# Kernel tuning notes

Measured on AMD Instinct MI355X. Metric: run time of the kernel, lower is better.

The kernel has to match this reference:

```python
import jax, jax.numpy as jnp
import numpy as np

N, E = 8192, 65536
IN_C, OUT_C, EF = 64, 16, 8
L1, L2 = 48, 32  # in - floor((in-out)/3), in - floor(2*(in-out)/3)


def setup_inputs() -> dict:
    key = jax.random.key(0)
    ks = jax.random.split(key, 10)
    rn = lambda k, shape, s: jax.random.normal(k, shape, dtype=jnp.float32) * s
    return {
        "x": jax.random.normal(ks[0], (N, IN_C), dtype=jnp.float32),
        "edge_index": jax.random.randint(ks[1], (2, E), 0, N, dtype=jnp.int32),
        "edge_attr": jax.random.normal(ks[2], (E, EF), dtype=jnp.float32),
        "nn1_w": rn(ks[3], (EF, IN_C * L1), 0.05),
        "nn1_b": jnp.zeros((IN_C * L1,), jnp.float32),
        "root1": rn(ks[4], (IN_C, L1), 0.1),
        "bias1": jnp.zeros((L1,), jnp.float32),
        "nn2_w": rn(ks[5], (EF, L1 * L2), 0.05),
        "nn2_b": jnp.zeros((L1 * L2,), jnp.float32),
        "root2": rn(ks[6], (L1, L2), 0.1),
        "bias2": jnp.zeros((L2,), jnp.float32),
        "mu_w": rn(ks[7], (L2, OUT_C), 0.1),
        "mu_b": jnp.zeros((OUT_C,), jnp.float32),
        "ls_w": rn(ks[8], (L2, OUT_C), 0.1),
        "ls_b": jnp.zeros((OUT_C,), jnp.float32),
    }


def _nnconv(x, src, dst, edge_attr, nn_w, nn_b, root, bias, c_in, c_out):
    # edge MLP -> per-edge weight matrices [E, c_in, c_out]
    w = (edge_attr @ nn_w + nn_b).reshape(-1, c_in, c_out)
    msg = jnp.einsum('ei,eio->eo', x[src], w)  # gather + per-edge matvec
    agg = jax.ops.segment_sum(msg, dst, num_segments=x.shape[0])  # sum aggregation
    return agg + x @ root + bias  # root transform + bias


def _gcn(x, src, dst, w, b):
    n = x.shape[0]
    # degree over target nodes, including self-loop (edge_weight = 1)
    deg = jax.ops.segment_sum(jnp.ones_like(src, jnp.float32), dst, num_segments=n) + 1.0
    dinv = jax.lax.rsqrt(deg)
    h = x @ w
    norm = dinv[src] * dinv[dst]  # [E]
    agg = jax.ops.segment_sum(h[src] * norm[:, None], dst, num_segments=n)
    return agg + h * (1.0 / deg)[:, None] + b  # self-loop contribution: deg_i^{-1}


def reference(x, edge_index, edge_attr, nn1_w, nn1_b, root1, bias1,
              nn2_w, nn2_b, root2, bias2, mu_w, mu_b, ls_w, ls_b):
    src, dst = edge_index[0], edge_index[1]
    h = jax.nn.relu(_nnconv(x, src, dst, edge_attr, nn1_w, nn1_b, root1, bias1, IN_C, L1))
    h = jax.nn.relu(_nnconv(h, src, dst, edge_attr, nn2_w, nn2_b, root2, bias2, L1, L2))
    return (_gcn(h, src, dst, mu_w, mu_b), _gcn(h, src, dst, ls_w, ls_b))
```

## Files before the change

kernel.cpp:

```cpp
#include <hip/hip_runtime.h>

#define NN 8192
#define EE 65536
#define IN_C 64
#define L1C 48
#define L2C 32
#define OUT_C 16
#define EF 8

#define T1_COLS 480
#define T2_COLS 320

__global__ __launch_bounds__(256) void k_T1(const float* __restrict__ x,
                                            const float* __restrict__ w,
                                            const float* __restrict__ b,
                                            const float* __restrict__ root,
                                            float* __restrict__ T1) {
    __shared__ float xsT[64 * 16];
    const int n0 = blockIdx.x * 16;
    for (int t = threadIdx.x; t < 16 * 64; t += 256) {
        int n = t >> 6, i = t & 63;
        xsT[i * 16 + n] = x[(n0 + n) * 64 + i];
    }
    __syncthreads();
    for (int c = threadIdx.x; c < T1_COLS; c += 256) {
        int f = c / 48, o = c - f * 48;
        const float* wp;
        if (f < 8)      wp = w + f * 3072 + o;
        else if (f == 8) wp = b + o;
        else             wp = root + o;
        float acc[16];
#pragma unroll
        for (int n = 0; n < 16; n++) acc[n] = 0.f;
#pragma unroll 16
        for (int i = 0; i < 64; i++) {
            float wv = wp[i * 48];
            const float* xr = &xsT[i * 16];
#pragma unroll
            for (int n = 0; n < 16; n++) acc[n] += xr[n] * wv;
        }
#pragma unroll
        for (int n = 0; n < 16; n++) T1[(size_t)(n0 + n) * T1_COLS + c] = acc[n];
    }
}

__global__ __launch_bounds__(256) void k_T2(const float* __restrict__ h1,
                                            const float* __restrict__ w,
                                            const float* __restrict__ b,
                                            const float* __restrict__ root,
                                            float* __restrict__ T2) {
    __shared__ float xsT[48 * 16];
    const int n0 = blockIdx.x * 16;
    for (int t = threadIdx.x; t < 16 * 48; t += 256) {
        int n = t / 48, i = t - n * 48;
        xsT[i * 16 + n] = h1[(n0 + n) * 48 + i];
    }
    __syncthreads();
    for (int c = threadIdx.x; c < T2_COLS; c += 256) {
        int f = c >> 5, o = c & 31;
        const float* wp;
        if (f < 8)      wp = w + f * 1536 + o;
        else if (f == 8) wp = b + o;
        else             wp = root + o;
        float acc[16];
#pragma unroll
        for (int n = 0; n < 16; n++) acc[n] = 0.f;
#pragma unroll 16
        for (int i = 0; i < 48; i++) {
            float wv = wp[i * 32];
            const float* xr = &xsT[i * 16];
#pragma unroll
            for (int n = 0; n < 16; n++) acc[n] += xr[n] * wv;
        }
#pragma unroll
        for (int n = 0; n < 16; n++) T2[(size_t)(n0 + n) * T2_COLS + c] = acc[n];
    }
}

__global__ __launch_bounds__(256) void k_zero(float* __restrict__ p, int n4) {
    int i = blockIdx.x * 256 + threadIdx.x;
    if (i < n4) ((float4*)p)[i] = make_float4(0.f, 0.f, 0.f, 0.f);
}

__global__ __launch_bounds__(256) void k_edge1(const int* __restrict__ ei,
                                               const float* __restrict__ ea,
                                               const float* __restrict__ T1,
                                               float* __restrict__ agg1) {
    int idx = blockIdx.x * 256 + threadIdx.x;
    int e = idx / 48, o = idx - e * 48;
    if (e >= EE) return;
    int s = ei[e], d = ei[EE + e];
    const float* t = T1 + (size_t)s * T1_COLS + o;
    const float4* a4 = (const float4*)(ea + (size_t)e * 8);
    float4 a0 = a4[0], a1 = a4[1];
    float m = t[384];
    m += a0.x * t[0 * 48];
    m += a0.y * t[1 * 48];
    m += a0.z * t[2 * 48];
    m += a0.w * t[3 * 48];
    m += a1.x * t[4 * 48];
    m += a1.y * t[5 * 48];
    m += a1.z * t[6 * 48];
    m += a1.w * t[7 * 48];
    atomicAdd(agg1 + (size_t)d * 48 + o, m);
}

__global__ __launch_bounds__(256) void k_h1(const float* __restrict__ agg1,
                                            const float* __restrict__ T1,
                                            const float* __restrict__ bias1,
                                            float* __restrict__ h1) {
    int idx = blockIdx.x * 256 + threadIdx.x;
    if (idx >= NN * 48) return;
    int n = idx / 48, o = idx - n * 48;
    float v = agg1[idx] + T1[(size_t)n * T1_COLS + 432 + o] + bias1[o];
    h1[idx] = v > 0.f ? v : 0.f;
}

__global__ __launch_bounds__(256) void k_edge2(const int* __restrict__ ei,
                                               const float* __restrict__ ea,
                                               const float* __restrict__ T2,
                                               float* __restrict__ agg2,
                                               float* __restrict__ deg) {
    int idx = blockIdx.x * 256 + threadIdx.x;
    int e = idx >> 5, o = idx & 31;
    if (e >= EE) return;
    int s = ei[e], d = ei[EE + e];
    const float* t = T2 + (size_t)s * T2_COLS + o;
    const float4* a4 = (const float4*)(ea + (size_t)e * 8);
    float4 a0 = a4[0], a1 = a4[1];
    float m = t[256];
    m += a0.x * t[0 * 32];
    m += a0.y * t[1 * 32];
    m += a0.z * t[2 * 32];
    m += a0.w * t[3 * 32];
    m += a1.x * t[4 * 32];
    m += a1.y * t[5 * 32];
    m += a1.z * t[6 * 32];
    m += a1.w * t[7 * 32];
    atomicAdd(agg2 + (size_t)d * 32 + o, m);
    if (o == 0) atomicAdd(deg + d, 1.0f);
}

__global__ __launch_bounds__(256) void k_post(const float* __restrict__ agg2,
                                              const float* __restrict__ T2,
                                              const float* __restrict__ bias2,
                                              const float* __restrict__ mu_w,
                                              const float* __restrict__ mu_b,
                                              const float* __restrict__ ls_w,
                                              const float* __restrict__ ls_b,
                                              const float* __restrict__ deg,
                                              float* __restrict__ hmu,
                                              float* __restrict__ hls,
                                              float* __restrict__ dinv,
                                              float* __restrict__ out) {
    __shared__ float h2s[8][32];
    const int n0 = blockIdx.x * 8;
    const int lid = threadIdx.x >> 5;
    const int o = threadIdx.x & 31;
    const int n = n0 + lid;
    float v = agg2[(size_t)n * 32 + o] + T2[(size_t)n * T2_COLS + 288 + o] + bias2[o];
    v = v > 0.f ? v : 0.f;
    h2s[lid][o] = v;
    __syncthreads();
    const float* wm = (o < 16) ? mu_w : ls_w;
    const float* bb = (o < 16) ? mu_b : ls_b;
    const int oo = o & 15;
    float acc = 0.f;
#pragma unroll
    for (int i = 0; i < 32; i++) acc += h2s[lid][i] * wm[i * 16 + oo];
    float d = deg[n] + 1.0f;
    float di = rsqrtf(d);
    if (o == 0) dinv[n] = di;
    float init = acc / d + bb[oo];
    if (o < 16) {
        hmu[(size_t)n * 16 + oo] = acc;
        out[(size_t)n * 16 + oo] = init;
    } else {
        hls[(size_t)n * 16 + oo] = acc;
        out[(size_t)NN * 16 + (size_t)n * 16 + oo] = init;
    }
}

__global__ __launch_bounds__(256) void k_gcn_edge(const int* __restrict__ ei,
                                                  const float* __restrict__ hmu,
                                                  const float* __restrict__ hls,
                                                  const float* __restrict__ dinv,
                                                  float* __restrict__ out) {
    int idx = blockIdx.x * 256 + threadIdx.x;
    int e = idx >> 4, o = idx & 15;
    if (e >= EE) return;
    int s = ei[e], d = ei[EE + e];
    float norm = dinv[s] * dinv[d];
    atomicAdd(out + (size_t)d * 16 + o, hmu[(size_t)s * 16 + o] * norm);
    atomicAdd(out + (size_t)NN * 16 + (size_t)d * 16 + o, hls[(size_t)s * 16 + o] * norm);
}

extern "C" void kernel_launch(void* const* d_in, const int* in_sizes, int n_in,
                              void* d_out, int out_size, void* d_ws, size_t ws_size,
                              hipStream_t stream) {
    const float* x     = (const float*)d_in[0];
    const int*   ei    = (const int*)d_in[1];
    const float* ea    = (const float*)d_in[2];
    const float* nn1_w = (const float*)d_in[3];
    const float* nn1_b = (const float*)d_in[4];
    const float* root1 = (const float*)d_in[5];
    const float* bias1 = (const float*)d_in[6];
    const float* nn2_w = (const float*)d_in[7];
    const float* nn2_b = (const float*)d_in[8];
    const float* root2 = (const float*)d_in[9];
    const float* bias2 = (const float*)d_in[10];
    const float* mu_w  = (const float*)d_in[11];
    const float* mu_b  = (const float*)d_in[12];
    const float* ls_w  = (const float*)d_in[13];
    const float* ls_b  = (const float*)d_in[14];
    float* out = (float*)d_out;

    float* W    = (float*)d_ws;
    float* T1   = W;
    float* T2   = W;
    float* agg1 = W + 3932160;
    float* agg2 = agg1 + 393216;
    float* deg  = agg2 + 262144;
    float* h1   = deg + 8192;
    float* hmu  = h1 + 393216;
    float* hls  = hmu + 131072;
    float* dinv = hls + 131072;

    k_T1<<<dim3(NN / 16), dim3(256), 0, stream>>>(x, nn1_w, nn1_b, root1, T1);
    k_zero<<<dim3((165888 + 255) / 256), dim3(256), 0, stream>>>(agg1, 165888);
    k_edge1<<<dim3((EE * 48) / 256), dim3(256), 0, stream>>>(ei, ea, T1, agg1);
    k_h1<<<dim3((NN * 48) / 256), dim3(256), 0, stream>>>(agg1, T1, bias1, h1);
    k_T2<<<dim3(NN / 16), dim3(256), 0, stream>>>(h1, nn2_w, nn2_b, root2, T2);
    k_edge2<<<dim3((EE * 32) / 256), dim3(256), 0, stream>>>(ei, ea, T2, agg2, deg);
    k_post<<<dim3(NN / 8), dim3(256), 0, stream>>>(agg2, T2, bias2, mu_w, mu_b,
                                                   ls_w, ls_b, deg, hmu, hls, dinv, out);
    k_gcn_edge<<<dim3((EE * 16) / 256), dim3(256), 0, stream>>>(ei, hmu, hls, dinv, out);
}
```

Before: 157.9 us.

## Prepack weights, fuse zero/ReLU kernels, vectorize edge kernels with float4

Adds a pre-kernel that zeroes the accumulators and repacks the edge-MLP, bias and root weights into contiguous row-major matrices. The node-transform GEMMs are restructured so each thread holds one node's features in registers and computes 32 output columns with uniform weight loads. The h1 ReLU kernel is fused into the T2 GEMM prologue, and T2 gets its own buffer instead of aliasing T1. The edge and GCN scatter kernels now use one thread per four channels with float4 gathers, cutting thread count and index loads, but they still issue scalar atomics and each thread carries more registers.

```diff
diff --git a/kernel.cpp b/kernel.cpp
--- a/kernel.cpp
+++ b/kernel.cpp
@@ -2,84 +2,116 @@
 
 #define NN 8192
 #define EE 65536
-#define IN_C 64
-#define L1C 48
-#define L2C 32
-#define OUT_C 16
-#define EF 8
-
 #define T1_COLS 480
 #define T2_COLS 320
 
+__global__ __launch_bounds__(256) void k_pre(const float* __restrict__ w1,
+                                             const float* __restrict__ b1,
+                                             const float* __restrict__ r1,
+                                             const float* __restrict__ w2,
+                                             const float* __restrict__ b2,
+                                             const float* __restrict__ r2,
+                                             float* __restrict__ Wp1,
+                                             float* __restrict__ Wp2,
+                                             float* __restrict__ zbase) {
+    int t = blockIdx.x * 256 + threadIdx.x;
+    if (t < 165888) {
+        ((float4*)zbase)[t] = make_float4(0.f, 0.f, 0.f, 0.f);
+        return;
+    }
+    int p = t - 165888;
+    if (p < 30720) {
+        int i = p / 480, c = p - i * 480;
+        float v;
+        if (c < 384) { int f = c / 48, o = c - f * 48; v = w1[f * 3072 + i * 48 + o]; }
+        else if (c < 432) v = b1[i * 48 + (c - 384)];
+        else              v = r1[i * 48 + (c - 432)];
+        Wp1[p] = v;
+    } else {
+        p -= 30720;
+        int i = p / 320, c = p - i * 320;
+        float v;
+        if (c < 256) { int f = c >> 5, o = c & 31; v = w2[f * 1536 + i * 32 + o]; }
+        else if (c < 288) v = b2[i * 32 + (c - 256)];
+        else              v = r2[i * 32 + (c - 288)];
+        Wp2[p] = v;
+    }
+}
+
 __global__ __launch_bounds__(256) void k_T1(const float* __restrict__ x,
-                                            const float* __restrict__ w,
-                                            const float* __restrict__ b,
-                                            const float* __restrict__ root,
+                                            const float* __restrict__ Wp,
                                             float* __restrict__ T1) {
-    __shared__ float xsT[64 * 16];
-    const int n0 = blockIdx.x * 16;
-    for (int t = threadIdx.x; t < 16 * 64; t += 256) {
-        int n = t >> 6, i = t & 63;
-        xsT[i * 16 + n] = x[(n0 + n) * 64 + i];
-    }
-    __syncthreads();
-    for (int c = threadIdx.x; c < T1_COLS; c += 256) {
-        int f = c / 48, o = c - f * 48;
-        const float* wp;
-        if (f < 8)      wp = w + f * 3072 + o;
-        else if (f == 8) wp = b + o;
-        else             wp = root + o;
+    const int j = blockIdx.x * 4 + (threadIdx.x >> 6);
+    const int lane = threadIdx.x & 63;
+    const int nt = j / 15, grp = j - nt * 15;
+    const int n = nt * 64 + lane;
+    float xr[64];
+    const float4* xp = (const float4*)(x + (size_t)n * 64);
+#pragma unroll
+    for (int q = 0; q < 16; q++) {
+        float4 v = xp[q];
+        xr[4 * q] = v.x; xr[4 * q + 1] = v.y; xr[4 * q + 2] = v.z; xr[4 * q + 3] = v.w;
+    }
+#pragma unroll
+    for (int ch = 0; ch < 2; ch++) {
+        const int c0 = grp * 32 + ch * 16;
+        const float* wr = Wp + c0;
         float acc[16];
 #pragma unroll
-        for (int n = 0; n < 16; n++) acc[n] = 0.f;
-#pragma unroll 16
+        for (int c = 0; c < 16; c++) acc[c] = 0.f;
+#pragma unroll
         for (int i = 0; i < 64; i++) {
-            float wv = wp[i * 48];
-            const float* xr = &xsT[i * 16];
-#pragma unroll
-            for (int n = 0; n < 16; n++) acc[n] += xr[n] * wv;
+            float xv = xr[i];
+#pragma unroll
+            for (int c = 0; c < 16; c++) acc[c] += xv * wr[i * 480 + c];
         }
-#pragma unroll
-        for (int n = 0; n < 16; n++) T1[(size_t)(n0 + n) * T1_COLS + c] = acc[n];
-    }
-}
-
-__global__ __launch_bounds__(256) void k_T2(const float* __restrict__ h1,
-                                            const float* __restrict__ w,
-                                            const float* __restrict__ b,
-                                            const float* __restrict__ root,
+        float4* o4 = (float4*)(T1 + (size_t)n * 480 + c0);
+#pragma unroll
+        for (int q = 0; q < 4; q++)
+            o4[q] = make_float4(acc[4 * q], acc[4 * q + 1], acc[4 * q + 2], acc[4 * q + 3]);
+    }
+}
+
+__global__ __launch_bounds__(256) void k_T2(const float* __restrict__ agg1,
+                                            const float* __restrict__ T1,
+                                            const float* __restrict__ bias1,
+                                            const float* __restrict__ Wp,
                                             float* __restrict__ T2) {
-    __shared__ float xsT[48 * 16];
-    const int n0 = blockIdx.x * 16;
-    for (int t = threadIdx.x; t < 16 * 48; t += 256) {
-        int n = t / 48, i = t - n * 48;
-        xsT[i * 16 + n] = h1[(n0 + n) * 48 + i];
-    }
-    __syncthreads();
-    for (int c = threadIdx.x; c < T2_COLS; c += 256) {
-        int f = c >> 5, o = c & 31;
-        const float* wp;
-        if (f < 8)      wp = w + f * 1536 + o;
-        else if (f == 8) wp = b + o;
-        else             wp = root + o;
+    const int j = blockIdx.x * 4 + (threadIdx.x >> 6);
+    const int lane = threadIdx.x & 63;
+    const int nt = j / 10, grp = j - nt * 10;
+    const int n = nt * 64 + lane;
+    float xr[48];
+    const float4* ap = (const float4*)(agg1 + (size_t)n * 48);
+    const float4* rp = (const float4*)(T1 + (size_t)n * 480 + 432);
+#pragma unroll
+    for (int q = 0; q < 12; q++) {
+        float4 a = ap[q];
+        float4 r = rp[q];
+        float4 b = *(const float4*)(bias1 + 4 * q);
+        xr[4 * q]     = fmaxf(a.x + r.x + b.x, 0.f);
+        xr[4 * q + 1] = fmaxf(a.y + r.y + b.y, 0.f);
+        xr[4 * q + 2] = fmaxf(a.z + r.z + b.z, 0.f);
+        xr[4 * q + 3] = fmaxf(a.w + r.w + b.w, 0.f);
+    }
+#pragma unroll
+    for (int ch = 0; ch < 2; ch++) {
+        const int c0 = grp * 32 + ch * 16;
+        const float* wr = Wp + c0;
         float acc[16];
 #pragma unroll
-        for (int n = 0; n < 16; n++) acc[n] = 0.f;
-#pragma unroll 16
+        for (int c = 0; c < 16; c++) acc[c] = 0.f;
+#pragma unroll
         for (int i = 0; i < 48; i++) {
-            float wv = wp[i * 32];
-            const float* xr = &xsT[i * 16];
-#pragma unroll
-            for (int n = 0; n < 16; n++) acc[n] += xr[n] * wv;
+            float xv = xr[i];
+#pragma unroll
+            for (int c = 0; c < 16; c++) acc[c] += xv * wr[i * 320 + c];
         }
-#pragma unroll
-        for (int n = 0; n < 16; n++) T2[(size_t)(n0 + n) * T2_COLS + c] = acc[n];
-    }
-}
-
-__global__ __launch_bounds__(256) void k_zero(float* __restrict__ p, int n4) {
-    int i = blockIdx.x * 256 + threadIdx.x;
-    if (i < n4) ((float4*)p)[i] = make_float4(0.f, 0.f, 0.f, 0.f);
+        float4* o4 = (float4*)(T2 + (size_t)n * 320 + c0);
+#pragma unroll
+        for (int q = 0; q < 4; q++)
+            o4[q] = make_float4(acc[4 * q], acc[4 * q + 1], acc[4 * q + 2], acc[4 * q + 3]);
+    }
 }
 
 __global__ __launch_bounds__(256) void k_edge1(const int* __restrict__ ei,
@@ -87,33 +119,27 @@
                                                const float* __restrict__ T1,
                                                float* __restrict__ agg1) {
     int idx = blockIdx.x * 256 + threadIdx.x;
-    int e = idx / 48, o = idx - e * 48;
+    int e = idx / 12, o4 = idx - e * 12;
     if (e >= EE) return;
     int s = ei[e], d = ei[EE + e];
-    const float* t = T1 + (size_t)s * T1_COLS + o;
+    const float* t = T1 + (size_t)s * 480 + o4 * 4;
     const float4* a4 = (const float4*)(ea + (size_t)e * 8);
     float4 a0 = a4[0], a1 = a4[1];
-    float m = t[384];
-    m += a0.x * t[0 * 48];
-    m += a0.y * t[1 * 48];
-    m += a0.z * t[2 * 48];
-    m += a0.w * t[3 * 48];
-    m += a1.x * t[4 * 48];
-    m += a1.y * t[5 * 48];
-    m += a1.z * t[6 * 48];
-    m += a1.w * t[7 * 48];
-    atomicAdd(agg1 + (size_t)d * 48 + o, m);
-}
-
-__global__ __launch_bounds__(256) void k_h1(const float* __restrict__ agg1,
-                                            const float* __restrict__ T1,
-                                            const float* __restrict__ bias1,
-                                            float* __restrict__ h1) {
-    int idx = blockIdx.x * 256 + threadIdx.x;
-    if (idx >= NN * 48) return;
-    int n = idx / 48, o = idx - n * 48;
-    float v = agg1[idx] + T1[(size_t)n * T1_COLS + 432 + o] + bias1[o];
-    h1[idx] = v > 0.f ? v : 0.f;
+    float4 m = *(const float4*)(t + 384);
+    float4 w;
+    w = *(const float4*)(t + 0 * 48); m.x += a0.x * w.x; m.y += a0.x * w.y; m.z += a0.x * w.z; m.w += a0.x * w.w;
+    w = *(const float4*)(t + 1 * 48); m.x += a0.y * w.x; m.y += a0.y * w.y; m.z += a0.y * w.z; m.w += a0.y * w.w;
+    w = *(const float4*)(t + 2 * 48); m.x += a0.z * w.x; m.y += a0.z * w.y; m.z += a0.z * w.z; m.w += a0.z * w.w;
+    w = *(const float4*)(t + 3 * 48); m.x += a0.w * w.x; m.y += a0.w * w.y; m.z += a0.w * w.z; m.w += a0.w * w.w;
+    w = *(const float4*)(t + 4 * 48); m.x += a1.x * w.x; m.y += a1.x * w.y; m.z += a1.x * w.z; m.w += a1.x * w.w;
+    w = *(const float4*)(t + 5 * 48); m.x += a1.y * w.x; m.y += a1.y * w.y; m.z += a1.y * w.z; m.w += a1.y * w.w;
+    w = *(const float4*)(t + 6 * 48); m.x += a1.z * w.x; m.y += a1.z * w.y; m.z += a1.z * w.z; m.w += a1.z * w.w;
+    w = *(const float4*)(t + 7 * 48); m.x += a1.w * w.x; m.y += a1.w * w.y; m.z += a1.w * w.z; m.w += a1.w * w.w;
+    float* ag = agg1 + (size_t)d * 48 + o4 * 4;
+    atomicAdd(ag + 0, m.x);
+    atomicAdd(ag + 1, m.y);
+    atomicAdd(ag + 2, m.z);
+    atomicAdd(ag + 3, m.w);
 }
 
 __global__ __launch_bounds__(256) void k_edge2(const int* __restrict__ ei,
@@ -122,23 +148,28 @@
                                                float* __restrict__ agg2,
                                                float* __restrict__ deg) {
     int idx = blockIdx.x * 256 + threadIdx.x;
-    int e = idx >> 5, o = idx & 31;
+    int e = idx >> 3, o4 = idx & 7;
     if (e >= EE) return;
     int s = ei[e], d = ei[EE + e];
-    const float* t = T2 + (size_t)s * T2_COLS + o;
+    const float* t = T2 + (size_t)s * 320 + o4 * 4;
     const float4* a4 = (const float4*)(ea + (size_t)e * 8);
     float4 a0 = a4[0], a1 = a4[1];
-    float m = t[256];
-    m += a0.x * t[0 * 32];
-    m += a0.y * t[1 * 32];
-    m += a0.z * t[2 * 32];
-    m += a0.w * t[3 * 32];
-    m += a1.x * t[4 * 32];
-    m += a1.y * t[5 * 32];
-    m += a1.z * t[6 * 32];
-    m += a1.w * t[7 * 32];
-    atomicAdd(agg2 + (size_t)d * 32 + o, m);
-    if (o == 0) atomicAdd(deg + d, 1.0f);
+    float4 m = *(const float4*)(t + 256);
+    float4 w;
+    w = *(const float4*)(t + 0 * 32); m.x += a0.x * w.x; m.y += a0.x * w.y; m.z += a0.x * w.z; m.w += a0.x * w.w;
+    w = *(const float4*)(t + 1 * 32); m.x += a0.y * w.x; m.y += a0.y * w.y; m.z += a0.y * w.z; m.w += a0.y * w.w;
+    w = *(const float4*)(t + 2 * 32); m.x += a0.z * w.x; m.y += a0.z * w.y; m.z += a0.z * w.z; m.w += a0.z * w.w;
+    w = *(const float4*)(t + 3 * 32); m.x += a0.w * w.x; m.y += a0.w * w.y; m.z += a0.w * w.z; m.w += a0.w * w.w;
+    w = *(const float4*)(t + 4 * 32); m.x += a1.x * w.x; m.y += a1.x * w.y; m.z += a1.x * w.z; m.w += a1.x * w.w;
+    w = *(const float4*)(t + 5 * 32); m.x += a1.y * w.x; m.y += a1.y * w.y; m.z += a1.y * w.z; m.w += a1.y * w.w;
+    w = *(const float4*)(t + 6 * 32); m.x += a1.z * w.x; m.y += a1.z * w.y; m.z += a1.z * w.z; m.w += a1.z * w.w;
+    w = *(const float4*)(t + 7 * 32); m.x += a1.w * w.x; m.y += a1.w * w.y; m.z += a1.w * w.z; m.w += a1.w * w.w;
+    float* ag = agg2 + (size_t)d * 32 + o4 * 4;
+    atomicAdd(ag + 0, m.x);
+    atomicAdd(ag + 1, m.y);
+    atomicAdd(ag + 2, m.z);
+    atomicAdd(ag + 3, m.w);
+    if (o4 == 0) atomicAdd(deg + d, 1.0f);
 }
 
 __global__ __launch_bounds__(256) void k_post(const float* __restrict__ agg2,
@@ -158,9 +189,8 @@
     const int lid = threadIdx.x >> 5;
     const int o = threadIdx.x & 31;
     const int n = n0 + lid;
-    float v = agg2[(size_t)n * 32 + o] + T2[(size_t)n * T2_COLS + 288 + o] + bias2[o];
-    v = v > 0.f ? v : 0.f;
-    h2s[lid][o] = v;
+    float v = agg2[(size_t)n * 32 + o] + T2[(size_t)n * 320 + 288 + o] + bias2[o];
+    h2s[lid][o] = v > 0.f ? v : 0.f;
     __syncthreads();
     const float* wm = (o < 16) ? mu_w : ls_w;
     const float* bb = (o < 16) ? mu_b : ls_b;
@@ -187,12 +217,22 @@
                                                   const float* __restrict__ dinv,
                                                   float* __restrict__ out) {
     int idx = blockIdx.x * 256 + threadIdx.x;
-    int e = idx >> 4, o = idx & 15;
+    int e = idx >> 2, o4 = idx & 3;
     if (e >= EE) return;
     int s = ei[e], d = ei[EE + e];
     float norm = dinv[s] * dinv[d];
-    atomicAdd(out + (size_t)d * 16 + o, hmu[(size_t)s * 16 + o] * norm);
-    atomicAdd(out + (size_t)NN * 16 + (size_t)d * 16 + o, hls[(size_t)s * 16 + o] * norm);
+    float4 m = *(const float4*)(hmu + (size_t)s * 16 + o4 * 4);
+    float4 l = *(const float4*)(hls + (size_t)s * 16 + o4 * 4);
+    float* om = out + (size_t)d * 16 + o4 * 4;
+    float* ol = out + (size_t)NN * 16 + (size_t)d * 16 + o4 * 4;
+    atomicAdd(om + 0, m.x * norm);
+    atomicAdd(om + 1, m.y * norm);
+    atomicAdd(om + 2, m.z * norm);
+    atomicAdd(om + 3, m.w * norm);
+    atomicAdd(ol + 0, l.x * norm);
+    atomicAdd(ol + 1, l.y * norm);
+    atomicAdd(ol + 2, l.z * norm);
+    atomicAdd(ol + 3, l.w * norm);
 }
 
 extern "C" void kernel_launch(void* const* d_in, const int* in_sizes, int n_in,
@@ -216,23 +256,25 @@
     float* out = (float*)d_out;
 
     float* W    = (float*)d_ws;
-    float* T1   = W;
-    float* T2   = W;
-    float* agg1 = W + 3932160;
+    float* Wp1  = W;
+    float* Wp2  = Wp1 + 30720;
+    float* T1   = Wp2 + 15360;
+    float* T2   = T1 + 3932160;
+    float* agg1 = T2 + 2621440;
     float* agg2 = agg1 + 393216;
     float* deg  = agg2 + 262144;
-    float* h1   = deg + 8192;
-    float* hmu  = h1 + 393216;
+    float* hmu  = deg + 8192;
     float* hls  = hmu + 131072;
     float* dinv = hls + 131072;
 
-    k_T1<<<dim3(NN / 16), dim3(256), 0, stream>>>(x, nn1_w, nn1_b, root1, T1);
-    k_zero<<<dim3((165888 + 255) / 256), dim3(256), 0, stream>>>(agg1, 165888);
-    k_edge1<<<dim3((EE * 48) / 256), dim3(256), 0, stream>>>(ei, ea, T1, agg1);
-    k_h1<<<dim3((NN * 48) / 256), dim3(256), 0, stream>>>(agg1, T1, bias1, h1);
-    k_T2<<<dim3(NN / 16), dim3(256), 0, stream>>>(h1, nn2_w, nn2_b, root2, T2);
-    k_edge2<<<dim3((EE * 32) / 256), dim3(256), 0, stream>>>(ei, ea, T2, agg2, deg);
+    k_pre<<<dim3(828), dim3(256), 0, stream>>>(nn1_w, nn1_b, root1,
+                                               nn2_w, nn2_b, root2,
+                                               Wp1, Wp2, agg1);
+    k_T1<<<dim3(480), dim3(256), 0, stream>>>(x, Wp1, T1);
+    k_edge1<<<dim3((EE * 12) / 256), dim3(256), 0, stream>>>(ei, ea, T1, agg1);
+    k_T2<<<dim3(320), dim3(256), 0, stream>>>(agg1, T1, bias1, Wp2, T2);
+    k_edge2<<<dim3((EE * 8) / 256), dim3(256), 0, stream>>>(ei, ea, T2, agg2, deg);
     k_post<<<dim3(NN / 8), dim3(256), 0, stream>>>(agg2, T2, bias2, mu_w, mu_b,
                                                    ls_w, ls_b, deg, hmu, hls, dinv, out);
-    k_gcn_edge<<<dim3((EE * 16) / 256), dim3(256), 0, stream>>>(ei, hmu, hls, dinv, out);
-}
+    k_gcn_edge<<<dim3((EE * 4) / 256), dim3(256), 0, stream>>>(ei, hmu, hls, dinv, out);
+}
```

Measured after the change: 274.7 us. 74.0% more time.

## Rebuild NNConv as CSR gather of edge-feature outer products then dense GEMM

Applied to the files above, without the earlier changes.

Replaces the atomic scatter pipeline with a CSR built on device (histogram, scan, scatter). Each NNConv first aggregates per-destination sums of edge_attr times source features (plus a plain sum and the self row), then applies one dense GEMM against the stacked weight, bias and root matrix. The GCN is also made atomic-free via CSR gather, and the mu/ls heads are fused with layer 2. This removes float atomics and the large per-source T tables, at the cost of several small extra kernels, including a single-block scan, and a large Z workspace.

```diff
diff --git a/kernel.cpp b/kernel.cpp
--- a/kernel.cpp
+++ b/kernel.cpp
@@ -2,197 +2,278 @@
 
 #define NN 8192
 #define EE 65536
-#define IN_C 64
-#define L1C 48
-#define L2C 32
-#define OUT_C 16
-#define EF 8
-
-#define T1_COLS 480
-#define T2_COLS 320
-
-__global__ __launch_bounds__(256) void k_T1(const float* __restrict__ x,
-                                            const float* __restrict__ w,
-                                            const float* __restrict__ b,
-                                            const float* __restrict__ root,
-                                            float* __restrict__ T1) {
-    __shared__ float xsT[64 * 16];
-    const int n0 = blockIdx.x * 16;
-    for (int t = threadIdx.x; t < 16 * 64; t += 256) {
-        int n = t >> 6, i = t & 63;
-        xsT[i * 16 + n] = x[(n0 + n) * 64 + i];
-    }
+
+__global__ __launch_bounds__(256) void k_pre(const float* __restrict__ w1,
+                                             const float* __restrict__ b1,
+                                             const float* __restrict__ r1,
+                                             const float* __restrict__ w2,
+                                             const float* __restrict__ b2,
+                                             const float* __restrict__ r2,
+                                             float* __restrict__ Wf1,
+                                             float* __restrict__ Wf2,
+                                             int* __restrict__ cnt) {
+    int t = blockIdx.x * 256 + threadIdx.x;
+    if (t < 8192) { cnt[t] = 0; return; }
+    t -= 8192;
+    if (t < 30720) {
+        float v;
+        if (t < 24576)      v = w1[t];
+        else if (t < 27648) v = b1[t - 24576];
+        else                v = r1[t - 27648];
+        Wf1[t] = v;
+        return;
+    }
+    t -= 30720;
+    float v;
+    if (t < 12288)      v = w2[t];
+    else if (t < 13824) v = b2[t - 12288];
+    else                v = r2[t - 13824];
+    Wf2[t] = v;
+}
+
+__global__ __launch_bounds__(256) void k_hist(const int* __restrict__ ei,
+                                              int* __restrict__ cnt) {
+    int e = blockIdx.x * 256 + threadIdx.x;
+    atomicAdd(&cnt[ei[EE + e]], 1);
+}
+
+__global__ __launch_bounds__(1024) void k_scan(const int* __restrict__ cnt,
+                                               int* __restrict__ row_ptr,
+                                               int* __restrict__ cursor) {
+    __shared__ int sd[1024];
+    const int t = threadIdx.x;
+    const int base = t * 8;
+    int v[8];
+    int s = 0;
+#pragma unroll
+    for (int j = 0; j < 8; j++) { v[j] = cnt[base + j]; s += v[j]; }
+    sd[t] = s;
     __syncthreads();
-    for (int c = threadIdx.x; c < T1_COLS; c += 256) {
-        int f = c / 48, o = c - f * 48;
-        const float* wp;
-        if (f < 8)      wp = w + f * 3072 + o;
-        else if (f == 8) wp = b + o;
-        else             wp = root + o;
-        float acc[16];
-#pragma unroll
-        for (int n = 0; n < 16; n++) acc[n] = 0.f;
-#pragma unroll 16
-        for (int i = 0; i < 64; i++) {
-            float wv = wp[i * 48];
-            const float* xr = &xsT[i * 16];
-#pragma unroll
-            for (int n = 0; n < 16; n++) acc[n] += xr[n] * wv;
-        }
-#pragma unroll
-        for (int n = 0; n < 16; n++) T1[(size_t)(n0 + n) * T1_COLS + c] = acc[n];
-    }
-}
-
-__global__ __launch_bounds__(256) void k_T2(const float* __restrict__ h1,
-                                            const float* __restrict__ w,
-                                            const float* __restrict__ b,
-                                            const float* __restrict__ root,
-                                            float* __restrict__ T2) {
-    __shared__ float xsT[48 * 16];
-    const int n0 = blockIdx.x * 16;
-    for (int t = threadIdx.x; t < 16 * 48; t += 256) {
-        int n = t / 48, i = t - n * 48;
-        xsT[i * 16 + n] = h1[(n0 + n) * 48 + i];
-    }
-    __syncthreads();
-    for (int c = threadIdx.x; c < T2_COLS; c += 256) {
-        int f = c >> 5, o = c & 31;
-        const float* wp;
-        if (f < 8)      wp = w + f * 1536 + o;
-        else if (f == 8) wp = b + o;
-        else             wp = root + o;
-        float acc[16];
-#pragma unroll
-        for (int n = 0; n < 16; n++) acc[n] = 0.f;
-#pragma unroll 16
-        for (int i = 0; i < 48; i++) {
-            float wv = wp[i * 32];
-            const float* xr = &xsT[i * 16];
-#pragma unroll
-            for (int n = 0; n < 16; n++) acc[n] += xr[n] * wv;
-        }
-#pragma unroll
-        for (int n = 0; n < 16; n++) T2[(size_t)(n0 + n) * T2_COLS + c] = acc[n];
-    }
-}
-
-__global__ __launch_bounds__(256) void k_zero(float* __restrict__ p, int n4) {
-    int i = blockIdx.x * 256 + threadIdx.x;
-    if (i < n4) ((float4*)p)[i] = make_float4(0.f, 0.f, 0.f, 0.f);
-}
-
-__global__ __launch_bounds__(256) void k_edge1(const int* __restrict__ ei,
-                                               const float* __restrict__ ea,
-                                               const float* __restrict__ T1,
-                                               float* __restrict__ agg1) {
-    int idx = blockIdx.x * 256 + threadIdx.x;
-    int e = idx / 48, o = idx - e * 48;
-    if (e >= EE) return;
-    int s = ei[e], d = ei[EE + e];
-    const float* t = T1 + (size_t)s * T1_COLS + o;
-    const float4* a4 = (const float4*)(ea + (size_t)e * 8);
-    float4 a0 = a4[0], a1 = a4[1];
-    float m = t[384];
-    m += a0.x * t[0 * 48];
-    m += a0.y * t[1 * 48];
-    m += a0.z * t[2 * 48];
-    m += a0.w * t[3 * 48];
-    m += a1.x * t[4 * 48];
-    m += a1.y * t[5 * 48];
-    m += a1.z * t[6 * 48];
-    m += a1.w * t[7 * 48];
-    atomicAdd(agg1 + (size_t)d * 48 + o, m);
-}
-
-__global__ __launch_bounds__(256) void k_h1(const float* __restrict__ agg1,
-                                            const float* __restrict__ T1,
+    for (int off = 1; off < 1024; off <<= 1) {
+        int a = sd[t];
+        int b = (t >= off) ? sd[t - off] : 0;
+        __syncthreads();
+        sd[t] = a + b;
+        __syncthreads();
+    }
+    int run = sd[t] - s;
+#pragma unroll
+    for (int j = 0; j < 8; j++) {
+        row_ptr[base + j] = run;
+        cursor[base + j] = run;
+        run += v[j];
+    }
+    if (t == 1023) row_ptr[8192] = run;
+}
+
+__global__ __launch_bounds__(256) void k_scatter(const int* __restrict__ ei,
+                                                 int* __restrict__ cursor,
+                                                 int* __restrict__ cs_e) {
+    int e = blockIdx.x * 256 + threadIdx.x;
+    int d = ei[EE + e];
+    int slot = atomicAdd(&cursor[d], 1);
+    cs_e[slot] = e;
+}
+
+__global__ __launch_bounds__(256) void k_y1(const int* __restrict__ ei,
+                                            const float* __restrict__ ea,
+                                            const float* __restrict__ x,
+                                            const int* __restrict__ row_ptr,
+                                            const int* __restrict__ cs_e,
+                                            float* __restrict__ Z1) {
+    const int lane = threadIdx.x & 63;
+    const int d = blockIdx.x * 4 + (threadIdx.x >> 6);
+    float y[9];
+#pragma unroll
+    for (int f = 0; f < 9; f++) y[f] = 0.f;
+    const int rp0 = row_ptr[d], rp1 = row_ptr[d + 1];
+    for (int idx = rp0; idx < rp1; idx++) {
+        int e = cs_e[idx];
+        int s = ei[e];
+        float xv = x[(size_t)s * 64 + lane];
+        float4 a0 = *(const float4*)(ea + (size_t)e * 8);
+        float4 a1 = *(const float4*)(ea + (size_t)e * 8 + 4);
+        y[0] += a0.x * xv; y[1] += a0.y * xv; y[2] += a0.z * xv; y[3] += a0.w * xv;
+        y[4] += a1.x * xv; y[5] += a1.y * xv; y[6] += a1.z * xv; y[7] += a1.w * xv;
+        y[8] += xv;
+    }
+    float* zr = Z1 + (size_t)d * 640;
+#pragma unroll
+    for (int f = 0; f < 9; f++) zr[f * 64 + lane] = y[f];
+    zr[576 + lane] = x[(size_t)d * 64 + lane];
+}
+
+__global__ __launch_bounds__(192) void k_g1(const float* __restrict__ Z1,
+                                            const float* __restrict__ Wf1,
                                             const float* __restrict__ bias1,
                                             float* __restrict__ h1) {
-    int idx = blockIdx.x * 256 + threadIdx.x;
-    if (idx >= NN * 48) return;
-    int n = idx / 48, o = idx - n * 48;
-    float v = agg1[idx] + T1[(size_t)n * T1_COLS + 432 + o] + bias1[o];
-    h1[idx] = v > 0.f ? v : 0.f;
-}
-
-__global__ __launch_bounds__(256) void k_edge2(const int* __restrict__ ei,
-                                               const float* __restrict__ ea,
-                                               const float* __restrict__ T2,
-                                               float* __restrict__ agg2,
-                                               float* __restrict__ deg) {
-    int idx = blockIdx.x * 256 + threadIdx.x;
-    int e = idx >> 5, o = idx & 31;
-    if (e >= EE) return;
-    int s = ei[e], d = ei[EE + e];
-    const float* t = T2 + (size_t)s * T2_COLS + o;
-    const float4* a4 = (const float4*)(ea + (size_t)e * 8);
-    float4 a0 = a4[0], a1 = a4[1];
-    float m = t[256];
-    m += a0.x * t[0 * 32];
-    m += a0.y * t[1 * 32];
-    m += a0.z * t[2 * 32];
-    m += a0.w * t[3 * 32];
-    m += a1.x * t[4 * 32];
-    m += a1.y * t[5 * 32];
-    m += a1.z * t[6 * 32];
-    m += a1.w * t[7 * 32];
-    atomicAdd(agg2 + (size_t)d * 32 + o, m);
-    if (o == 0) atomicAdd(deg + d, 1.0f);
-}
-
-__global__ __launch_bounds__(256) void k_post(const float* __restrict__ agg2,
-                                              const float* __restrict__ T2,
-                                              const float* __restrict__ bias2,
-                                              const float* __restrict__ mu_w,
-                                              const float* __restrict__ mu_b,
-                                              const float* __restrict__ ls_w,
-                                              const float* __restrict__ ls_b,
-                                              const float* __restrict__ deg,
-                                              float* __restrict__ hmu,
-                                              float* __restrict__ hls,
-                                              float* __restrict__ dinv,
-                                              float* __restrict__ out) {
-    __shared__ float h2s[8][32];
-    const int n0 = blockIdx.x * 8;
-    const int lid = threadIdx.x >> 5;
-    const int o = threadIdx.x & 31;
-    const int n = n0 + lid;
-    float v = agg2[(size_t)n * 32 + o] + T2[(size_t)n * T2_COLS + 288 + o] + bias2[o];
-    v = v > 0.f ? v : 0.f;
-    h2s[lid][o] = v;
+    __shared__ float Zs[64 * 32];
+    __shared__ float Ws[64 * 48];
+    const int t = threadIdx.x;
+    const int nb = blockIdx.x * 32;
+    const int n0 = (t & 7) * 4;
+    const int c0 = (t >> 3) * 2;
+    float acc[4][2] = {{0.f, 0.f}, {0.f, 0.f}, {0.f, 0.f}, {0.f, 0.f}};
+    for (int k0 = 0; k0 < 640; k0 += 64) {
+        for (int idx = t; idx < 512; idx += 192) {
+            int nn = idx >> 4, kk = (idx & 15) * 4;
+            float4 v = *(const float4*)(Z1 + (size_t)(nb + nn) * 640 + k0 + kk);
+            Zs[(kk + 0) * 32 + nn] = v.x;
+            Zs[(kk + 1) * 32 + nn] = v.y;
+            Zs[(kk + 2) * 32 + nn] = v.z;
+            Zs[(kk + 3) * 32 + nn] = v.w;
+        }
+        for (int idx = t; idx < 768; idx += 192) {
+            *(float4*)(Ws + idx * 4) = *(const float4*)(Wf1 + (size_t)k0 * 48 + idx * 4);
+        }
+        __syncthreads();
+#pragma unroll 8
+        for (int k = 0; k < 64; k++) {
+            float4 a = *(const float4*)(Zs + k * 32 + n0);
+            float2 w = *(const float2*)(Ws + k * 48 + c0);
+            acc[0][0] += a.x * w.x; acc[0][1] += a.x * w.y;
+            acc[1][0] += a.y * w.x; acc[1][1] += a.y * w.y;
+            acc[2][0] += a.z * w.x; acc[2][1] += a.z * w.y;
+            acc[3][0] += a.w * w.x; acc[3][1] += a.w * w.y;
+        }
+        __syncthreads();
+    }
+    float2 b = *(const float2*)(bias1 + c0);
+#pragma unroll
+    for (int i = 0; i < 4; i++) {
+        int n = nb + n0 + i;
+        float2 o;
+        o.x = fmaxf(acc[i][0] + b.x, 0.f);
+        o.y = fmaxf(acc[i][1] + b.y, 0.f);
+        *(float2*)(h1 + (size_t)n * 48 + c0) = o;
+    }
+}
+
+__global__ __launch_bounds__(256) void k_y2(const int* __restrict__ ei,
+                                            const float* __restrict__ ea,
+                                            const float* __restrict__ h1,
+                                            const int* __restrict__ row_ptr,
+                                            const int* __restrict__ cs_e,
+                                            float* __restrict__ Z2) {
+    const int lane = threadIdx.x & 63;
+    const int d = blockIdx.x * 4 + (threadIdx.x >> 6);
+    if (lane >= 48) return;
+    float y[9];
+#pragma unroll
+    for (int f = 0; f < 9; f++) y[f] = 0.f;
+    const int rp0 = row_ptr[d], rp1 = row_ptr[d + 1];
+    for (int idx = rp0; idx < rp1; idx++) {
+        int e = cs_e[idx];
+        int s = ei[e];
+        float hv = h1[(size_t)s * 48 + lane];
+        float4 a0 = *(const float4*)(ea + (size_t)e * 8);
+        float4 a1 = *(const float4*)(ea + (size_t)e * 8 + 4);
+        y[0] += a0.x * hv; y[1] += a0.y * hv; y[2] += a0.z * hv; y[3] += a0.w * hv;
+        y[4] += a1.x * hv; y[5] += a1.y * hv; y[6] += a1.z * hv; y[7] += a1.w * hv;
+        y[8] += hv;
+    }
+    float* zr = Z2 + (size_t)d * 480;
+#pragma unroll
+    for (int f = 0; f < 9; f++) zr[f * 48 + lane] = y[f];
+    zr[432 + lane] = h1[(size_t)d * 48 + lane];
+}
+
+__global__ __launch_bounds__(256) void k_g2(const float* __restrict__ Z2,
+                                            const float* __restrict__ Wf2,
+                                            const float* __restrict__ bias2,
+                                            const float* __restrict__ mu_w,
+                                            const float* __restrict__ mu_b,
+                                            const float* __restrict__ ls_w,
+                                            const float* __restrict__ ls_b,
+                                            const int* __restrict__ row_ptr,
+                                            float* __restrict__ hcat,
+                                            float* __restrict__ dinv,
+                                            float* __restrict__ out) {
+    __shared__ float Zs[48 * 32];
+    __shared__ float Ws[48 * 32];
+    __shared__ float h2s[32 * 33];
+    const int t = threadIdx.x;
+    const int nb = blockIdx.x * 32;
+    const int n0 = (t & 15) * 2;
+    const int c0 = (t >> 4) * 2;
+    float acc[2][2] = {{0.f, 0.f}, {0.f, 0.f}};
+    for (int k0 = 0; k0 < 480; k0 += 48) {
+        for (int idx = t; idx < 384; idx += 256) {
+            int nn = idx / 12, kk = (idx % 12) * 4;
+            float4 v = *(const float4*)(Z2 + (size_t)(nb + nn) * 480 + k0 + kk);
+            Zs[(kk + 0) * 32 + nn] = v.x;
+            Zs[(kk + 1) * 32 + nn] = v.y;
+            Zs[(kk + 2) * 32 + nn] = v.z;
+            Zs[(kk + 3) * 32 + nn] = v.w;
+        }
+        for (int idx = t; idx < 384; idx += 256) {
+            *(float4*)(Ws + idx * 4) = *(const float4*)(Wf2 + (size_t)k0 * 32 + idx * 4);
+        }
+        __syncthreads();
+#pragma unroll 8
+        for (int k = 0; k < 48; k++) {
+            float2 a = *(const float2*)(Zs + k * 32 + n0);
+            float2 w = *(const float2*)(Ws + k * 32 + c0);
+            acc[0][0] += a.x * w.x; acc[0][1] += a.x * w.y;
+            acc[1][0] += a.y * w.x; acc[1][1] += a.y * w.y;
+        }
+        __syncthreads();
+    }
+    float2 b2v = *(const float2*)(bias2 + c0);
+    h2s[(n0 + 0) * 33 + c0]     = fmaxf(acc[0][0] + b2v.x, 0.f);
+    h2s[(n0 + 0) * 33 + c0 + 1] = fmaxf(acc[0][1] + b2v.y, 0.f);
+    h2s[(n0 + 1) * 33 + c0]     = fmaxf(acc[1][0] + b2v.x, 0.f);
+    h2s[(n0 + 1) * 33 + c0 + 1] = fmaxf(acc[1][1] + b2v.y, 0.f);
     __syncthreads();
-    const float* wm = (o < 16) ? mu_w : ls_w;
-    const float* bb = (o < 16) ? mu_b : ls_b;
-    const int oo = o & 15;
+    const int n = t >> 3;
+    const int q = t & 7;
+    const float* wh = (q < 4) ? mu_w : ls_w;
+    const float* bh = (q < 4) ? mu_b : ls_b;
+    const int base_o = (q & 3) * 4;
+    float a4[4] = {0.f, 0.f, 0.f, 0.f};
+#pragma unroll 8
+    for (int i = 0; i < 32; i++) {
+        float v = h2s[n * 33 + i];
+        a4[0] += v * wh[i * 16 + base_o + 0];
+        a4[1] += v * wh[i * 16 + base_o + 1];
+        a4[2] += v * wh[i * 16 + base_o + 2];
+        a4[3] += v * wh[i * 16 + base_o + 3];
+    }
+    const int d = nb + n;
+    const int degi = row_ptr[d + 1] - row_ptr[d] + 1;
+    const float invd = 1.f / (float)degi;
+    if (q == 0) dinv[d] = rsqrtf((float)degi);
+    const size_t outbase = (q < 4) ? 0 : (size_t)NN * 16;
+    const int hoff = (q < 4) ? 0 : 16;
+#pragma unroll
+    for (int j = 0; j < 4; j++) {
+        int col = base_o + j;
+        hcat[(size_t)d * 32 + hoff + col] = a4[j];
+        out[outbase + (size_t)d * 16 + col] = a4[j] * invd + bh[col];
+    }
+}
+
+__global__ __launch_bounds__(256) void k_gcn(const int* __restrict__ ei,
+                                             const int* __restrict__ row_ptr,
+                                             const int* __restrict__ cs_e,
+                                             const float* __restrict__ hcat,
+                                             const float* __restrict__ dinv,
+                                             float* __restrict__ out) {
+    const int t = threadIdx.x;
+    const int lane32 = t & 31;
+    const int d = blockIdx.x * 8 + (t >> 5);
     float acc = 0.f;
-#pragma unroll
-    for (int i = 0; i < 32; i++) acc += h2s[lid][i] * wm[i * 16 + oo];
-    float d = deg[n] + 1.0f;
-    float di = rsqrtf(d);
-    if (o == 0) dinv[n] = di;
-    float init = acc / d + bb[oo];
-    if (o < 16) {
-        hmu[(size_t)n * 16 + oo] = acc;
-        out[(size_t)n * 16 + oo] = init;
-    } else {
-        hls[(size_t)n * 16 + oo] = acc;
-        out[(size_t)NN * 16 + (size_t)n * 16 + oo] = init;
-    }
-}
-
-__global__ __launch_bounds__(256) void k_gcn_edge(const int* __restrict__ ei,
-                                                  const float* __restrict__ hmu,
-                                                  const float* __restrict__ hls,
-                                                  const float* __restrict__ dinv,
-                                                  float* __restrict__ out) {
-    int idx = blockIdx.x * 256 + threadIdx.x;
-    int e = idx >> 4, o = idx & 15;
-    if (e >= EE) return;
-    int s = ei[e], d = ei[EE + e];
-    float norm = dinv[s] * dinv[d];
-    atomicAdd(out + (size_t)d * 16 + o, hmu[(size_t)s * 16 + o] * norm);
-    atomicAdd(out + (size_t)NN * 16 + (size_t)d * 16 + o, hls[(size_t)s * 16 + o] * norm);
+    const int rp0 = row_ptr[d], rp1 = row_ptr[d + 1];
+    for (int idx = rp0; idx < rp1; idx++) {
+        int e = cs_e[idx];
+        int s = ei[e];
+        acc += hcat[(size_t)s * 32 + lane32] * dinv[s];
+    }
+    acc *= dinv[d];
+    const int col = lane32 & 15;
+    const size_t addr = (lane32 < 16) ? ((size_t)d * 16 + col)
+                                      : ((size_t)NN * 16 + (size_t)d * 16 + col);
+    out[addr] += acc;
 }
 
 extern "C" void kernel_launch(void* const* d_in, const int* in_sizes, int n_in,
@@ -215,24 +296,29 @@
     const float* ls_b  = (const float*)d_in[14];
     float* out = (float*)d_out;
 
-    float* W    = (float*)d_ws;
-    float* T1   = W;
-    float* T2   = W;
-    float* agg1 = W + 3932160;
-    float* agg2 = agg1 + 393216;
-    float* deg  = agg2 + 262144;
-    float* h1   = deg + 8192;
-    float* hmu  = h1 + 393216;
-    float* hls  = hmu + 131072;
-    float* dinv = hls + 131072;
-
-    k_T1<<<dim3(NN / 16), dim3(256), 0, stream>>>(x, nn1_w, nn1_b, root1, T1);
-    k_zero<<<dim3((165888 + 255) / 256), dim3(256), 0, stream>>>(agg1, 165888);
-    k_edge1<<<dim3((EE * 48) / 256), dim3(256), 0, stream>>>(ei, ea, T1, agg1);
-    k_h1<<<dim3((NN * 48) / 256), dim3(256), 0, stream>>>(agg1, T1, bias1, h1);
-    k_T2<<<dim3(NN / 16), dim3(256), 0, stream>>>(h1, nn2_w, nn2_b, root2, T2);
-    k_edge2<<<dim3((EE * 32) / 256), dim3(256), 0, stream>>>(ei, ea, T2, agg2, deg);
-    k_post<<<dim3(NN / 8), dim3(256), 0, stream>>>(agg2, T2, bias2, mu_w, mu_b,
-                                                   ls_w, ls_b, deg, hmu, hls, dinv, out);
-    k_gcn_edge<<<dim3((EE * 16) / 256), dim3(256), 0, stream>>>(ei, hmu, hls, dinv, out);
-}
+    float* W      = (float*)d_ws;
+    float* Wf1    = W;
+    float* Wf2    = Wf1 + 30720;
+    int*   cnt    = (int*)(Wf2 + 15360);
+    int*   row_ptr= cnt + 8192;
+    int*   cursor = row_ptr + 8196;
+    int*   cs_e   = cursor + 8192;
+    float* Z1     = (float*)(cs_e + 65536);
+    float* Z2     = Z1 + 5242880;
+    float* h1     = Z2 + 3932160;
+    float* hcat   = h1 + 393216;
+    float* dinv   = hcat + 262144;
+
+    k_pre<<<dim3(212), dim3(256), 0, stream>>>(nn1_w, nn1_b, root1,
+                                               nn2_w, nn2_b, root2,
+                                               Wf1, Wf2, cnt);
+    k_hist<<<dim3(256), dim3(256), 0, stream>>>(ei, cnt);
+    k_scan<<<dim3(1), dim3(1024), 0, stream>>>(cnt, row_ptr, cursor);
+    k_scatter<<<dim3(256), dim3(256), 0, stream>>>(ei, cursor, cs_e);
+    k_y1<<<dim3(2048), dim3(256), 0, stream>>>(ei, ea, x, row_ptr, cs_e, Z1);
+    k_g1<<<dim3(256), dim3(192), 0, stream>>>(Z1, Wf1, bias1, h1);
+    k_y2<<<dim3(2048), dim3(256), 0, stream>>>(ei, ea, h1, row_ptr, cs_e, Z2);
+    k_g2<<<dim3(256), dim3(256), 0, stream>>>(Z2, Wf2, bias2, mu_w, mu_b,
+                                              ls_w, ls_b, row_ptr, hcat, dinv, out);
+    k_gcn<<<dim3(1024), dim3(256), 0, stream>>>(ei, row_ptr, cs_e, hcat, dinv, out);
+}
```

Measured after the change: 204.1 us. 1.29x slower.
